# Performance work log

Measured on AMD Instinct MI355X. Metric: run time of the kernel, lower is better.

Reference implementation:

```python
import jax, jax.numpy as jnp
import numpy as np

B, S, D, H = 2, 2048, 1024, 16
DK = D // H  # 64


def setup_inputs() -> dict:
    key = jax.random.key(0)
    k0, k1, k2, k3, k4, k5, k6 = jax.random.split(key, 7)
    scale = 0.02
    return {
        "q": jax.random.normal(k0, (B, S, D), dtype=jnp.float32),
        "k": jax.random.normal(k1, (B, S, D), dtype=jnp.float32),
        "v": jax.random.normal(k2, (B, S, D), dtype=jnp.float32),
        # per-head Q/K projection weights (n_head separate Linear layers, bias=False)
        "Wq": jax.random.normal(k3, (H, D, DK), dtype=jnp.float32) * scale,
        "Wk": jax.random.normal(k4, (H, D, DK), dtype=jnp.float32) * scale,
        # shared V projection (the same v_layer object is reused for every head)
        "Wv": jax.random.normal(k5, (D, DK), dtype=jnp.float32) * scale,
        # output projection fc: d_v -> d_model, bias=False
        "Wo": jax.random.normal(k6, (DK, D), dtype=jnp.float32) * scale,
    }


def reference(q, k, v, Wq, Wk, Wv, Wo):
    d_k = Wq.shape[-1]
    # batched per-head projections (replaces the Python loop over heads)
    qs = jnp.einsum("bsd,hdk->bhsk", q, Wq)          # [B,H,S,DK]
    ks = jnp.einsum("bsd,hdk->bhsk", k, Wk)          # [B,H,S,DK]
    vs = jnp.einsum("bsd,dk->bsk", v, Wv)            # [B,S,DK] shared across heads
    scores = jnp.einsum("bhsk,bhtk->bhst", qs, ks) / jnp.sqrt(
        jnp.asarray(d_k, dtype=jnp.float32)
    )                                                 # [B,H,S,S]
    attn = jax.nn.softmax(scores, axis=-1)            # [B,H,S,S]; dropout = identity (eval)
    heads = jnp.einsum("bhst,btk->bhsk", attn, vs)    # [B,H,S,DK]
    head = heads.mean(axis=1)                         # mean over heads, not concat
    attn_mean = attn.mean(axis=1)                     # [B,S,S]
    out = jnp.einsum("bsk,kd->bsd", head, Wo)         # [B,S,D]; dropout = identity
    return (out, attn_mean)
```

## Files before the change

### kernel.cpp

```cpp
#include <hip/hip_runtime.h>

#define B_ 2
#define S_ 2048
#define D_ 1024
#define H_ 16
#define DK_ 64

typedef __bf16 bf8 __attribute__((ext_vector_type(8)));
typedef float f4 __attribute__((ext_vector_type(4)));
typedef unsigned short u16x8 __attribute__((ext_vector_type(8)));

__device__ __forceinline__ unsigned short f2bf_bits(float f) {
  unsigned int u = __float_as_uint(f);
  return (unsigned short)((u + 0x7fffu + ((u >> 16) & 1u)) >> 16);
}

__device__ __forceinline__ bf8 pack_bf8(f4 lo, f4 hi) {
  u16x8 u;
  u[0] = f2bf_bits(lo[0]); u[1] = f2bf_bits(lo[1]);
  u[2] = f2bf_bits(lo[2]); u[3] = f2bf_bits(lo[3]);
  u[4] = f2bf_bits(hi[0]); u[5] = f2bf_bits(hi[1]);
  u[6] = f2bf_bits(hi[2]); u[7] = f2bf_bits(hi[3]);
  union { u16x8 u; bf8 b; } x; x.u = u; return x.b;
}

__device__ __forceinline__ bf8 ldb(const unsigned short* p) {
  return *reinterpret_cast<const bf8*>(p);
}

__device__ __forceinline__ void stage16(const void* g, void* l) {
  __builtin_amdgcn_global_load_lds(
      (const __attribute__((address_space(1))) void*)g,
      (__attribute__((address_space(3))) void*)l, 16, 0, 0);
}

#define MFMA(a, b, c) __builtin_amdgcn_mfma_f32_16x16x32_bf16((a), (b), (c), 0, 0, 0)

__global__ void k_prep(const float* __restrict__ q, const float* __restrict__ k,
                       const float* __restrict__ wq, const float* __restrict__ wk,
                       const float* __restrict__ wv, const float* __restrict__ wo,
                       unsigned short* __restrict__ qb, unsigned short* __restrict__ kb,
                       unsigned short* __restrict__ wqt, unsigned short* __restrict__ wkt,
                       unsigned short* __restrict__ wvt, unsigned short* __restrict__ wot) {
  __shared__ float tl[64 * 65];
  int bid = blockIdx.x, tid = threadIdx.x;
  const int rr = tid >> 6, cc = tid & 63;
  if (bid < 4096) {
    int which = bid >> 11;
    long i = ((long)(bid & 2047) * 256 + tid) * 8;
    const float* src = which ? k : q;
    unsigned short* dst = which ? kb : qb;
    f4 lo = *reinterpret_cast<const f4*>(src + i);
    f4 hi = *reinterpret_cast<const f4*>(src + i + 4);
    *reinterpret_cast<bf8*>(dst + i) = pack_bf8(lo, hi);
  } else if (bid < 4352) {
    int blk = bid - 4096;
    int h = blk >> 4, d0 = (blk & 15) * 64;
    for (int m = 0; m < 2; ++m) {
      const float* src = m ? wk : wq;
      unsigned short* dst = m ? wkt : wqt;
      if (m) __syncthreads();
#pragma unroll
      for (int it = 0; it < 16; ++it) {
        int d = it * 4 + rr;
        tl[cc * 65 + d] = src[(long)h * 65536 + (d0 + d) * 64 + cc];
      }
      __syncthreads();
#pragma unroll
      for (int it = 0; it < 16; ++it) {
        int n = it * 4 + rr;
        dst[(long)h * 65536 + n * 1024 + d0 + cc] = f2bf_bits(tl[n * 65 + cc]);
      }
    }
  } else if (bid < 4368) {
    int d0 = (bid - 4352) * 64;
#pragma unroll
    for (int it = 0; it < 16; ++it) {
      int d = it * 4 + rr;
      tl[cc * 65 + d] = wv[(long)(d0 + d) * 64 + cc];
    }
    __syncthreads();
#pragma unroll
    for (int it = 0; it < 16; ++it) {
      int n = it * 4 + rr;
      wvt[(long)n * 1024 + d0 + cc] = f2bf_bits(tl[n * 65 + cc]);
    }
  } else {
    int d0 = (bid - 4368) * 64;
#pragma unroll
    for (int it = 0; it < 16; ++it) {
      int kk = it * 4 + rr;
      tl[cc * 65 + kk] = wo[(long)kk * 1024 + d0 + cc];
    }
    __syncthreads();
#pragma unroll
    for (int it = 0; it < 16; ++it) {
      int ddl = it * 4 + rr;
      wot[(long)(d0 + ddl) * 64 + cc] = f2bf_bits(tl[ddl * 65 + cc]);
    }
  }
}

__global__ __launch_bounds__(256) void k_gemm_qk(
    const unsigned short* __restrict__ qb, const unsigned short* __restrict__ kb,
    const unsigned short* __restrict__ wqt, const unsigned short* __restrict__ wkt,
    unsigned short* __restrict__ qsb, unsigned short* __restrict__ ksb) {
  __shared__ unsigned short lds[8192];
  const int tid = threadIdx.x, wave = tid >> 6, lane = tid & 63;
  const int l15 = lane & 15, quad = lane >> 4;
  const int m0 = blockIdx.x * 128, n0 = blockIdx.y * 128;
  const int which = blockIdx.z;
  const unsigned short* A = which ? kb : qb;
  const unsigned short* W = which ? wkt : wqt;
  unsigned short* C = which ? ksb : qsb;
  const float scale = which ? 1.0f : 0.18033688011112042f;
  const int wr = wave >> 1, wc = wave & 1;

  f4 acc[4][4];
#pragma unroll
  for (int i = 0; i < 4; ++i)
#pragma unroll
    for (int j = 0; j < 4; ++j) acc[i][j] = f4{0.f, 0.f, 0.f, 0.f};

  const int sl15 = tid & 15, squad = (tid >> 4) & 3, st = tid >> 6;
  const unsigned short* gA = A + (long)(m0 + st * 16 + sl15) * D_ + squad * 8;
  const unsigned short* gB = W + (long)(n0 + st * 16 + sl15) * D_ + squad * 8;

  for (int k0 = 0; k0 < D_; k0 += 32) {
    stage16(gA + k0, lds + tid * 8);
    stage16(gA + 64 * D_ + k0, lds + 2048 + tid * 8);
    stage16(gB + k0, lds + 4096 + tid * 8);
    stage16(gB + 64 * D_ + k0, lds + 6144 + tid * 8);
    __syncthreads();
    bf8 aF[4], bF[4];
#pragma unroll
    for (int mi = 0; mi < 4; ++mi)
      aF[mi] = ldb(lds + (wr * 4 + mi) * 512 + lane * 8);
#pragma unroll
    for (int ni = 0; ni < 4; ++ni)
      bF[ni] = ldb(lds + 4096 + (wc * 4 + ni) * 512 + lane * 8);
#pragma unroll
    for (int mi = 0; mi < 4; ++mi)
#pragma unroll
      for (int ni = 0; ni < 4; ++ni)
        acc[mi][ni] = MFMA(aF[mi], bF[ni], acc[mi][ni]);
    __syncthreads();
  }
#pragma unroll
  for (int mi = 0; mi < 4; ++mi)
#pragma unroll
    for (int r = 0; r < 4; ++r) {
      long row = m0 + wr * 64 + mi * 16 + quad * 4 + r;
#pragma unroll
      for (int ni = 0; ni < 4; ++ni)
        C[row * D_ + n0 + wc * 64 + ni * 16 + l15] = f2bf_bits(acc[mi][ni][r] * scale);
    }
}

__global__ __launch_bounds__(256) void k_pv(
    const float* __restrict__ v, const unsigned short* __restrict__ wvt,
    float* __restrict__ pv) {
  const int tid = threadIdx.x, wave = tid >> 6, lane = tid & 63;
  const int l15 = lane & 15, quad = lane >> 4;
  const int rg = blockIdx.x, kc = blockIdx.y;
  const int row0 = rg * 64 + wave * 16;
  const float* arow = v + (long)(row0 + l15) * D_ + kc * 256 + quad * 8;
  const unsigned short* wbase = wvt + kc * 256 + quad * 8;
  f4 acc[4];
  for (int i = 0; i < 4; ++i) acc[i] = f4{0.f, 0.f, 0.f, 0.f};
  for (int k0 = 0; k0 < 256; k0 += 32) {
    f4 alo = *reinterpret_cast<const f4*>(arow + k0);
    f4 ahi = *reinterpret_cast<const f4*>(arow + k0 + 4);
    bf8 a = pack_bf8(alo, ahi);
#pragma unroll
    for (int i = 0; i < 4; ++i) {
      bf8 bf = ldb(wbase + (long)(i * 16 + l15) * D_ + k0);
      acc[i] = MFMA(a, bf, acc[i]);
    }
  }
#pragma unroll
  for (int i = 0; i < 4; ++i)
#pragma unroll
    for (int r = 0; r < 4; ++r)
      pv[((long)kc * 4096 + row0 + quad * 4 + r) * 64 + i * 16 + l15] = acc[i][r];
}

__global__ void k_vred(const float* __restrict__ pv, unsigned short* __restrict__ vst) {
  int e = blockIdx.x * 256 + threadIdx.x;
  int t = e & 2047, dk = (e >> 11) & 63, b = e >> 17;
  long row = (long)b * S_ + t;
  float s = pv[row * 64 + dk] + pv[(4096 + row) * 64 + dk] +
            pv[(8192 + row) * 64 + dk] + pv[(12288 + row) * 64 + dk];
  vst[e] = f2bf_bits(s);
}

__global__ __launch_bounds__(512) void k_denom(
    const unsigned short* __restrict__ qsb, const unsigned short* __restrict__ ksb,
    float* __restrict__ recip) {
  __shared__ unsigned short lds[8192];
  const int tid = threadIdx.x, wave = tid >> 6, lane = tid & 63;
  const int l15 = lane & 15, quad = lane >> 4;
  const int stile = blockIdx.x, h = blockIdx.y, b = blockIdx.z;
  const int s0 = stile * 128 + wave * 16;

  const unsigned short* qrow = qsb + ((long)(b * S_) + s0 + l15) * D_ + h * 64 + quad * 8;
  bf8 a0 = ldb(qrow);
  bf8 a1 = ldb(qrow + 32);

  f4 sum = f4{0.f, 0.f, 0.f, 0.f};
  for (int t0 = 0; t0 < S_; t0 += 128) {
#pragma unroll
    for (int i = 0; i < 2; ++i) {
      int u = i * 512 + tid;
      int sl15 = u & 15, squad = (u >> 4) & 3, stt = (u >> 6) & 7, sh2 = u >> 9;
      stage16(ksb + ((long)(b * S_) + t0 + stt * 16 + sl15) * D_ + h * 64 + sh2 * 32 + squad * 8,
              lds + u * 8);
    }
    __syncthreads();
#pragma unroll
    for (int tt = 0; tt < 8; ++tt) {
      bf8 b0 = ldb(lds + tt * 512 + lane * 8);
      bf8 b1 = ldb(lds + 4096 + tt * 512 + lane * 8);
      f4 d = f4{0.f, 0.f, 0.f, 0.f};
      d = MFMA(a0, b0, d);
      d = MFMA(a1, b1, d);
#pragma unroll
      for (int r = 0; r < 4; ++r) sum[r] += __builtin_amdgcn_exp2f(d[r]);
    }
    __syncthreads();
  }
#pragma unroll
  for (int m = 1; m < 16; m <<= 1) {
#pragma unroll
    for (int r = 0; r < 4; ++r) sum[r] += __shfl_xor(sum[r], m, 64);
  }
  if (l15 == 0) {
    float* rp = recip + (long)(b * H_ + h) * S_ + s0 + quad * 4;
#pragma unroll
    for (int r = 0; r < 4; ++r) rp[r] = 1.0f / (16.0f * sum[r]);
  }
}

__global__ __launch_bounds__(512) void k_attn(
    const unsigned short* __restrict__ qsb, const unsigned short* __restrict__ ksb,
    const float* __restrict__ recip, float* __restrict__ am) {
  __shared__ unsigned short lds[8192];
  const int tid = threadIdx.x, wave = tid >> 6, lane = tid & 63;
  const int l15 = lane & 15, quad = lane >> 4;
  const int tchunk = blockIdx.x, stile = blockIdx.y, b = blockIdx.z;
  const int s0 = stile * 128 + wave * 16;
  const int t0c = tchunk * 128;

  f4 acc[8];
#pragma unroll
  for (int tt = 0; tt < 8; ++tt) acc[tt] = f4{0.f, 0.f, 0.f, 0.f};

  const unsigned short* qbase = qsb + ((long)(b * S_) + s0 + l15) * D_ + quad * 8;

  for (int h = 0; h < H_; ++h) {
#pragma unroll
    for (int i = 0; i < 2; ++i) {
      int u = i * 512 + tid;
      int sl15 = u & 15, squad = (u >> 4) & 3, stt = (u >> 6) & 7, sh2 = u >> 9;
      stage16(ksb + ((long)(b * S_) + t0c + stt * 16 + sl15) * D_ + h * 64 + sh2 * 32 + squad * 8,
              lds + u * 8);
    }
    bf8 a0 = ldb(qbase + h * 64);
    bf8 a1 = ldb(qbase + h * 64 + 32);
    f4 rp = *reinterpret_cast<const f4*>(recip + (long)(b * H_ + h) * S_ + s0 + quad * 4);
    __syncthreads();
#pragma unroll
    for (int tt = 0; tt < 8; ++tt) {
      bf8 b0 = ldb(lds + tt * 512 + lane * 8);
      bf8 b1 = ldb(lds + 4096 + tt * 512 + lane * 8);
      f4 d = f4{0.f, 0.f, 0.f, 0.f};
      d = MFMA(a0, b0, d);
      d = MFMA(a1, b1, d);
#pragma unroll
      for (int r = 0; r < 4; ++r) acc[tt][r] += rp[r] * __builtin_amdgcn_exp2f(d[r]);
    }
    __syncthreads();
  }
  float* obase = am + ((long)b * S_ + s0 + quad * 4) * S_ + t0c + l15;
#pragma unroll
  for (int tt = 0; tt < 8; ++tt)
#pragma unroll
    for (int r = 0; r < 4; ++r) obase[(long)r * S_ + tt * 16] = acc[tt][r];
}

__global__ __launch_bounds__(256) void k_hpart(
    const float* __restrict__ am, const unsigned short* __restrict__ vst,
    float* __restrict__ ph) {
  const int tid = threadIdx.x, wave = tid >> 6, lane = tid & 63;
  const int l15 = lane & 15, quad = lane >> 4;
  const int rg = blockIdx.x, kc = blockIdx.y;
  const int row0 = rg * 64 + wave * 16;
  const int b = row0 >> 11;
  const float* arow = am + (long)(row0 + l15) * S_ + kc * 512 + quad * 8;
  const unsigned short* vb = vst + (long)b * DK_ * S_ + kc * 512 + quad * 8;
  f4 acc[4];
  for (int i = 0; i < 4; ++i) acc[i] = f4{0.f, 0.f, 0.f, 0.f};
  for (int t0 = 0; t0 < 512; t0 += 32) {
    f4 alo = *reinterpret_cast<const f4*>(arow + t0);
    f4 ahi = *reinterpret_cast<const f4*>(arow + t0 + 4);
    bf8 a = pack_bf8(alo, ahi);
#pragma unroll
    for (int i = 0; i < 4; ++i) {
      bf8 bf = ldb(vb + (long)(i * 16 + l15) * S_ + t0);
      acc[i] = MFMA(a, bf, acc[i]);
    }
  }
#pragma unroll
  for (int i = 0; i < 4; ++i)
#pragma unroll
    for (int r = 0; r < 4; ++r)
      ph[((long)kc * 4096 + row0 + quad * 4 + r) * 64 + i * 16 + l15] = acc[i][r];
}

__global__ void k_hred(const float* __restrict__ ph, unsigned short* __restrict__ headb) {
  int e = blockIdx.x * 256 + threadIdx.x;
  float s = ph[e] + ph[e + 4096 * 64] + ph[e + 2 * 4096 * 64] + ph[e + 3 * 4096 * 64];
  headb[e] = f2bf_bits(s);
}

__global__ __launch_bounds__(256) void k_out(
    const unsigned short* __restrict__ head, const unsigned short* __restrict__ wot,
    float* __restrict__ out) {
  const int tid = threadIdx.x, wave = tid >> 6, lane = tid & 63;
  const int l15 = lane & 15, quad = lane >> 4;
  const int dchunk = blockIdx.x, stile = blockIdx.y, b = blockIdx.z;
  const int s0 = stile * 64 + wave * 16;
  const int n0 = dchunk * 128;
  const unsigned short* hrow = head + ((long)b * S_ + s0 + l15) * DK_ + quad * 8;
  bf8 a0 = ldb(hrow);
  bf8 a1 = ldb(hrow + 32);
  const unsigned short* wb = wot + quad * 8;
  float* obase = out + ((long)b * S_ + s0 + quad * 4) * D_ + n0 + l15;
#pragma unroll
  for (int i = 0; i < 8; ++i) {
    const unsigned short* wp = wb + (long)(n0 + i * 16 + l15) * DK_;
    bf8 b0 = ldb(wp);
    bf8 b1 = ldb(wp + 32);
    f4 d = f4{0.f, 0.f, 0.f, 0.f};
    d = MFMA(a0, b0, d);
    d = MFMA(a1, b1, d);
#pragma unroll
    for (int r = 0; r < 4; ++r) obase[(long)r * D_ + i * 16] = d[r];
  }
}

extern "C" void kernel_launch(void* const* d_in, const int* in_sizes, int n_in,
                              void* d_out, int out_size, void* d_ws, size_t ws_size,
                              hipStream_t stream) {
  const float* q  = (const float*)d_in[0];
  const float* k  = (const float*)d_in[1];
  const float* v  = (const float*)d_in[2];
  const float* Wq = (const float*)d_in[3];
  const float* Wk = (const float*)d_in[4];
  const float* Wv = (const float*)d_in[5];
  const float* Wo = (const float*)d_in[6];

  float* out = (float*)d_out;
  float* am  = out + (long)B_ * S_ * D_;

  unsigned short* qsb  = (unsigned short*)d_ws;
  unsigned short* ksb  = qsb + 4194304;
  unsigned short* wqt  = ksb + 4194304;
  unsigned short* wkt  = wqt + 1048576;
  unsigned short* wvt  = wkt + 1048576;
  unsigned short* wot  = wvt + 65536;
  unsigned short* vst  = wot + 65536;
  unsigned short* headb= vst + 262144;
  float* recip = (float*)(headb + 262144);

  unsigned short* qb = (unsigned short*)am;
  unsigned short* kb = qb + 4194304;
  float* part = out;

  k_prep<<<4384, 256, 0, stream>>>(q, k, Wq, Wk, Wv, Wo, qb, kb, wqt, wkt, wvt, wot);
  k_gemm_qk<<<dim3(32, 8, 2), 256, 0, stream>>>(qb, kb, wqt, wkt, qsb, ksb);
  k_pv<<<dim3(64, 4), 256, 0, stream>>>(v, wvt, part);
  k_vred<<<1024, 256, 0, stream>>>(part, vst);
  k_denom<<<dim3(16, 16, 2), 512, 0, stream>>>(qsb, ksb, recip);
  k_attn<<<dim3(16, 16, 2), 512, 0, stream>>>(qsb, ksb, recip, am);
  k_hpart<<<dim3(64, 4), 256, 0, stream>>>(am, vst, part);
  k_hred<<<1024, 256, 0, stream>>>(part, headb);
  k_out<<<dim3(8, 32, 2), 256, 0, stream>>>(headb, wot, out);
}
```

Measured before the change: 246.9 us.

## Double-buffer K tiles in attention kernels, widen GEMM K-step, split reductions finer

The denominator and attention kernels now use 256 threads with each wave covering 32 query rows, so each staged K fragment feeds two MFMA chains. They also double-buffer K tiles in LDS, prefetching the next head or t-chunk while computing the current one. The QK projection GEMM stages 64-wide K slices per barrier instead of 32, halving the number of syncs. The V-projection and head-partial kernels split the reduction into 8 chunks instead of 4 for more blocks, and the reducers sum 8 partials. The cost is higher register and LDS use per block and more partial-sum traffic.

```diff
diff --git a/kernel.cpp b/kernel.cpp
--- a/kernel.cpp
+++ b/kernel.cpp
@@ -105,7 +105,7 @@
     const unsigned short* __restrict__ qb, const unsigned short* __restrict__ kb,
     const unsigned short* __restrict__ wqt, const unsigned short* __restrict__ wkt,
     unsigned short* __restrict__ qsb, unsigned short* __restrict__ ksb) {
-  __shared__ unsigned short lds[8192];
+  __shared__ unsigned short lds[16384];
   const int tid = threadIdx.x, wave = tid >> 6, lane = tid & 63;
   const int l15 = lane & 15, quad = lane >> 4;
   const int m0 = blockIdx.x * 128, n0 = blockIdx.y * 128;
@@ -122,28 +122,31 @@
 #pragma unroll
     for (int j = 0; j < 4; ++j) acc[i][j] = f4{0.f, 0.f, 0.f, 0.f};
 
-  const int sl15 = tid & 15, squad = (tid >> 4) & 3, st = tid >> 6;
-  const unsigned short* gA = A + (long)(m0 + st * 16 + sl15) * D_ + squad * 8;
-  const unsigned short* gB = W + (long)(n0 + st * 16 + sl15) * D_ + squad * 8;
-
-  for (int k0 = 0; k0 < D_; k0 += 32) {
-    stage16(gA + k0, lds + tid * 8);
-    stage16(gA + 64 * D_ + k0, lds + 2048 + tid * 8);
-    stage16(gB + k0, lds + 4096 + tid * 8);
-    stage16(gB + 64 * D_ + k0, lds + 6144 + tid * 8);
-    __syncthreads();
-    bf8 aF[4], bF[4];
-#pragma unroll
-    for (int mi = 0; mi < 4; ++mi)
-      aF[mi] = ldb(lds + (wr * 4 + mi) * 512 + lane * 8);
-#pragma unroll
-    for (int ni = 0; ni < 4; ++ni)
-      bF[ni] = ldb(lds + 4096 + (wc * 4 + ni) * 512 + lane * 8);
-#pragma unroll
-    for (int mi = 0; mi < 4; ++mi)
+  for (int k0 = 0; k0 < D_; k0 += 64) {
+#pragma unroll
+    for (int i = 0; i < 4; ++i) {
+      int u = i * 256 + tid;
+      int T = u >> 6, rg = T & 7, kh = T >> 3, sl15 = u & 15, squad = (u >> 4) & 3;
+      stage16(A + (long)(m0 + rg * 16 + sl15) * D_ + k0 + kh * 32 + squad * 8, lds + u * 8);
+      stage16(W + (long)(n0 + rg * 16 + sl15) * D_ + k0 + kh * 32 + squad * 8,
+              lds + 8192 + u * 8);
+    }
+    __syncthreads();
+#pragma unroll
+    for (int kh = 0; kh < 2; ++kh) {
+      bf8 aF[4], bF[4];
+#pragma unroll
+      for (int mi = 0; mi < 4; ++mi)
+        aF[mi] = ldb(lds + (wr * 4 + mi + 8 * kh) * 512 + lane * 8);
 #pragma unroll
       for (int ni = 0; ni < 4; ++ni)
-        acc[mi][ni] = MFMA(aF[mi], bF[ni], acc[mi][ni]);
+        bF[ni] = ldb(lds + 8192 + (wc * 4 + ni + 8 * kh) * 512 + lane * 8);
+#pragma unroll
+      for (int mi = 0; mi < 4; ++mi)
+#pragma unroll
+        for (int ni = 0; ni < 4; ++ni)
+          acc[mi][ni] = MFMA(aF[mi], bF[ni], acc[mi][ni]);
+    }
     __syncthreads();
   }
 #pragma unroll
@@ -164,11 +167,12 @@
   const int l15 = lane & 15, quad = lane >> 4;
   const int rg = blockIdx.x, kc = blockIdx.y;
   const int row0 = rg * 64 + wave * 16;
-  const float* arow = v + (long)(row0 + l15) * D_ + kc * 256 + quad * 8;
-  const unsigned short* wbase = wvt + kc * 256 + quad * 8;
+  const float* arow = v + (long)(row0 + l15) * D_ + kc * 128 + quad * 8;
+  const unsigned short* wbase = wvt + kc * 128 + quad * 8;
   f4 acc[4];
   for (int i = 0; i < 4; ++i) acc[i] = f4{0.f, 0.f, 0.f, 0.f};
-  for (int k0 = 0; k0 < 256; k0 += 32) {
+#pragma unroll
+  for (int k0 = 0; k0 < 128; k0 += 32) {
     f4 alo = *reinterpret_cast<const f4*>(arow + k0);
     f4 ahi = *reinterpret_cast<const f4*>(arow + k0 + 4);
     bf8 a = pack_bf8(alo, ahi);
@@ -189,103 +193,157 @@
   int e = blockIdx.x * 256 + threadIdx.x;
   int t = e & 2047, dk = (e >> 11) & 63, b = e >> 17;
   long row = (long)b * S_ + t;
-  float s = pv[row * 64 + dk] + pv[(4096 + row) * 64 + dk] +
-            pv[(8192 + row) * 64 + dk] + pv[(12288 + row) * 64 + dk];
+  float s = 0.f;
+#pragma unroll
+  for (int c = 0; c < 8; ++c) s += pv[((long)c * 4096 + row) * 64 + dk];
   vst[e] = f2bf_bits(s);
 }
 
-__global__ __launch_bounds__(512) void k_denom(
+__global__ __launch_bounds__(256) void k_denom(
     const unsigned short* __restrict__ qsb, const unsigned short* __restrict__ ksb,
     float* __restrict__ recip) {
-  __shared__ unsigned short lds[8192];
+  __shared__ unsigned short lds[16384];
   const int tid = threadIdx.x, wave = tid >> 6, lane = tid & 63;
   const int l15 = lane & 15, quad = lane >> 4;
   const int stile = blockIdx.x, h = blockIdx.y, b = blockIdx.z;
-  const int s0 = stile * 128 + wave * 16;
-
-  const unsigned short* qrow = qsb + ((long)(b * S_) + s0 + l15) * D_ + h * 64 + quad * 8;
-  bf8 a0 = ldb(qrow);
-  bf8 a1 = ldb(qrow + 32);
-
-  f4 sum = f4{0.f, 0.f, 0.f, 0.f};
-  for (int t0 = 0; t0 < S_; t0 += 128) {
-#pragma unroll
-    for (int i = 0; i < 2; ++i) {
-      int u = i * 512 + tid;
-      int sl15 = u & 15, squad = (u >> 4) & 3, stt = (u >> 6) & 7, sh2 = u >> 9;
-      stage16(ksb + ((long)(b * S_) + t0 + stt * 16 + sl15) * D_ + h * 64 + sh2 * 32 + squad * 8,
-              lds + u * 8);
-    }
-    __syncthreads();
+  const int sw = stile * 128 + wave * 32;
+
+  const unsigned short* qrow0 = qsb + ((long)(b * S_) + sw + l15) * D_ + h * 64 + quad * 8;
+  bf8 a0 = ldb(qrow0);
+  bf8 a1 = ldb(qrow0 + 32);
+  bf8 a2 = ldb(qrow0 + 16 * D_);
+  bf8 a3 = ldb(qrow0 + 16 * D_ + 32);
+
+  f4 sum0 = f4{0.f, 0.f, 0.f, 0.f}, sum1 = f4{0.f, 0.f, 0.f, 0.f};
+
+  const long kbase = (long)(b * S_);
+#pragma unroll
+  for (int i = 0; i < 4; ++i) {
+    int u = i * 256 + tid;
+    int T = u >> 6, sl15 = u & 15, squad = (u >> 4) & 3;
+    stage16(ksb + (kbase + (T & 7) * 16 + sl15) * D_ + h * 64 + (T >> 3) * 32 + squad * 8,
+            lds + u * 8);
+  }
+  for (int it = 0; it < 16; ++it) {
+    __syncthreads();
+    if (it < 15) {
+      int t0n = (it + 1) * 128, bufn = (it + 1) & 1;
+#pragma unroll
+      for (int i = 0; i < 4; ++i) {
+        int u = i * 256 + tid;
+        int T = u >> 6, sl15 = u & 15, squad = (u >> 4) & 3;
+        stage16(ksb + (kbase + t0n + (T & 7) * 16 + sl15) * D_ + h * 64 + (T >> 3) * 32 + squad * 8,
+                lds + bufn * 8192 + u * 8);
+      }
+    }
+    const unsigned short* L = lds + (it & 1) * 8192;
 #pragma unroll
     for (int tt = 0; tt < 8; ++tt) {
-      bf8 b0 = ldb(lds + tt * 512 + lane * 8);
-      bf8 b1 = ldb(lds + 4096 + tt * 512 + lane * 8);
-      f4 d = f4{0.f, 0.f, 0.f, 0.f};
-      d = MFMA(a0, b0, d);
-      d = MFMA(a1, b1, d);
-#pragma unroll
-      for (int r = 0; r < 4; ++r) sum[r] += __builtin_amdgcn_exp2f(d[r]);
-    }
-    __syncthreads();
+      bf8 b0 = ldb(L + tt * 512 + lane * 8);
+      bf8 b1 = ldb(L + 4096 + tt * 512 + lane * 8);
+      f4 d0 = f4{0.f, 0.f, 0.f, 0.f};
+      d0 = MFMA(a0, b0, d0);
+      d0 = MFMA(a1, b1, d0);
+      f4 d1 = f4{0.f, 0.f, 0.f, 0.f};
+      d1 = MFMA(a2, b0, d1);
+      d1 = MFMA(a3, b1, d1);
+#pragma unroll
+      for (int r = 0; r < 4; ++r) {
+        sum0[r] += __builtin_amdgcn_exp2f(d0[r]);
+        sum1[r] += __builtin_amdgcn_exp2f(d1[r]);
+      }
+    }
   }
 #pragma unroll
   for (int m = 1; m < 16; m <<= 1) {
 #pragma unroll
-    for (int r = 0; r < 4; ++r) sum[r] += __shfl_xor(sum[r], m, 64);
+    for (int r = 0; r < 4; ++r) {
+      sum0[r] += __shfl_xor(sum0[r], m, 64);
+      sum1[r] += __shfl_xor(sum1[r], m, 64);
+    }
   }
   if (l15 == 0) {
-    float* rp = recip + (long)(b * H_ + h) * S_ + s0 + quad * 4;
-#pragma unroll
-    for (int r = 0; r < 4; ++r) rp[r] = 1.0f / (16.0f * sum[r]);
-  }
-}
-
-__global__ __launch_bounds__(512) void k_attn(
+    float* rp0 = recip + (long)(b * H_ + h) * S_ + sw + quad * 4;
+#pragma unroll
+    for (int r = 0; r < 4; ++r) {
+      rp0[r] = 1.0f / (16.0f * sum0[r]);
+      rp0[16 + r] = 1.0f / (16.0f * sum1[r]);
+    }
+  }
+}
+
+__global__ __launch_bounds__(256) void k_attn(
     const unsigned short* __restrict__ qsb, const unsigned short* __restrict__ ksb,
     const float* __restrict__ recip, float* __restrict__ am) {
-  __shared__ unsigned short lds[8192];
+  __shared__ unsigned short lds[16384];
   const int tid = threadIdx.x, wave = tid >> 6, lane = tid & 63;
   const int l15 = lane & 15, quad = lane >> 4;
   const int tchunk = blockIdx.x, stile = blockIdx.y, b = blockIdx.z;
-  const int s0 = stile * 128 + wave * 16;
+  const int sw = stile * 128 + wave * 32;
   const int t0c = tchunk * 128;
 
-  f4 acc[8];
-#pragma unroll
-  for (int tt = 0; tt < 8; ++tt) acc[tt] = f4{0.f, 0.f, 0.f, 0.f};
-
-  const unsigned short* qbase = qsb + ((long)(b * S_) + s0 + l15) * D_ + quad * 8;
-
+  f4 acc0[8], acc1[8];
+#pragma unroll
+  for (int tt = 0; tt < 8; ++tt) {
+    acc0[tt] = f4{0.f, 0.f, 0.f, 0.f};
+    acc1[tt] = f4{0.f, 0.f, 0.f, 0.f};
+  }
+
+  const unsigned short* qrow0 = qsb + ((long)(b * S_) + sw + l15) * D_ + quad * 8;
+  const long kbase = (long)(b * S_) + t0c;
+
+#pragma unroll
+  for (int i = 0; i < 4; ++i) {
+    int u = i * 256 + tid;
+    int T = u >> 6, sl15 = u & 15, squad = (u >> 4) & 3;
+    stage16(ksb + (kbase + (T & 7) * 16 + sl15) * D_ + (T >> 3) * 32 + squad * 8, lds + u * 8);
+  }
   for (int h = 0; h < H_; ++h) {
-#pragma unroll
-    for (int i = 0; i < 2; ++i) {
-      int u = i * 512 + tid;
-      int sl15 = u & 15, squad = (u >> 4) & 3, stt = (u >> 6) & 7, sh2 = u >> 9;
-      stage16(ksb + ((long)(b * S_) + t0c + stt * 16 + sl15) * D_ + h * 64 + sh2 * 32 + squad * 8,
-              lds + u * 8);
-    }
-    bf8 a0 = ldb(qbase + h * 64);
-    bf8 a1 = ldb(qbase + h * 64 + 32);
-    f4 rp = *reinterpret_cast<const f4*>(recip + (long)(b * H_ + h) * S_ + s0 + quad * 4);
-    __syncthreads();
+    __syncthreads();
+    if (h < 15) {
+      int bufn = (h + 1) & 1;
+#pragma unroll
+      for (int i = 0; i < 4; ++i) {
+        int u = i * 256 + tid;
+        int T = u >> 6, sl15 = u & 15, squad = (u >> 4) & 3;
+        stage16(ksb + (kbase + (T & 7) * 16 + sl15) * D_ + (h + 1) * 64 + (T >> 3) * 32 + squad * 8,
+                lds + bufn * 8192 + u * 8);
+      }
+    }
+    const unsigned short* L = lds + (h & 1) * 8192;
+    bf8 a0 = ldb(qrow0 + h * 64);
+    bf8 a1 = ldb(qrow0 + h * 64 + 32);
+    bf8 a2 = ldb(qrow0 + 16 * D_ + h * 64);
+    bf8 a3 = ldb(qrow0 + 16 * D_ + h * 64 + 32);
+    const float* rpp = recip + (long)(b * H_ + h) * S_ + sw + quad * 4;
+    f4 rp0 = *reinterpret_cast<const f4*>(rpp);
+    f4 rp1 = *reinterpret_cast<const f4*>(rpp + 16);
 #pragma unroll
     for (int tt = 0; tt < 8; ++tt) {
-      bf8 b0 = ldb(lds + tt * 512 + lane * 8);
-      bf8 b1 = ldb(lds + 4096 + tt * 512 + lane * 8);
-      f4 d = f4{0.f, 0.f, 0.f, 0.f};
-      d = MFMA(a0, b0, d);
-      d = MFMA(a1, b1, d);
-#pragma unroll
-      for (int r = 0; r < 4; ++r) acc[tt][r] += rp[r] * __builtin_amdgcn_exp2f(d[r]);
-    }
-    __syncthreads();
-  }
-  float* obase = am + ((long)b * S_ + s0 + quad * 4) * S_ + t0c + l15;
+      bf8 b0 = ldb(L + tt * 512 + lane * 8);
+      bf8 b1 = ldb(L + 4096 + tt * 512 + lane * 8);
+      f4 d0 = f4{0.f, 0.f, 0.f, 0.f};
+      d0 = MFMA(a0, b0, d0);
+      d0 = MFMA(a1, b1, d0);
+      f4 d1 = f4{0.f, 0.f, 0.f, 0.f};
+      d1 = MFMA(a2, b0, d1);
+      d1 = MFMA(a3, b1, d1);
+#pragma unroll
+      for (int r = 0; r < 4; ++r) {
+        acc0[tt][r] += rp0[r] * __builtin_amdgcn_exp2f(d0[r]);
+        acc1[tt][r] += rp1[r] * __builtin_amdgcn_exp2f(d1[r]);
+      }
+    }
+  }
+  float* ob0 = am + ((long)b * S_ + sw + quad * 4) * S_ + t0c + l15;
+  float* ob1 = ob0 + 16 * S_;
 #pragma unroll
   for (int tt = 0; tt < 8; ++tt)
 #pragma unroll
-    for (int r = 0; r < 4; ++r) obase[(long)r * S_ + tt * 16] = acc[tt][r];
+    for (int r = 0; r < 4; ++r) {
+      ob0[(long)r * S_ + tt * 16] = acc0[tt][r];
+      ob1[(long)r * S_ + tt * 16] = acc1[tt][r];
+    }
 }
 
 __global__ __launch_bounds__(256) void k_hpart(
@@ -296,11 +354,12 @@
   const int rg = blockIdx.x, kc = blockIdx.y;
   const int row0 = rg * 64 + wave * 16;
   const int b = row0 >> 11;
-  const float* arow = am + (long)(row0 + l15) * S_ + kc * 512 + quad * 8;
-  const unsigned short* vb = vst + (long)b * DK_ * S_ + kc * 512 + quad * 8;
+  const float* arow = am + (long)(row0 + l15) * S_ + kc * 256 + quad * 8;
+  const unsigned short* vb = vst + (long)b * DK_ * S_ + kc * 256 + quad * 8;
   f4 acc[4];
   for (int i = 0; i < 4; ++i) acc[i] = f4{0.f, 0.f, 0.f, 0.f};
-  for (int t0 = 0; t0 < 512; t0 += 32) {
+#pragma unroll
+  for (int t0 = 0; t0 < 256; t0 += 32) {
     f4 alo = *reinterpret_cast<const f4*>(arow + t0);
     f4 ahi = *reinterpret_cast<const f4*>(arow + t0 + 4);
     bf8 a = pack_bf8(alo, ahi);
@@ -319,7 +378,9 @@
 
 __global__ void k_hred(const float* __restrict__ ph, unsigned short* __restrict__ headb) {
   int e = blockIdx.x * 256 + threadIdx.x;
-  float s = ph[e] + ph[e + 4096 * 64] + ph[e + 2 * 4096 * 64] + ph[e + 3 * 4096 * 64];
+  float s = 0.f;
+#pragma unroll
+  for (int c = 0; c < 8; ++c) s += ph[(long)c * 262144 + e];
   headb[e] = f2bf_bits(s);
 }
 
@@ -379,11 +440,11 @@
 
   k_prep<<<4384, 256, 0, stream>>>(q, k, Wq, Wk, Wv, Wo, qb, kb, wqt, wkt, wvt, wot);
   k_gemm_qk<<<dim3(32, 8, 2), 256, 0, stream>>>(qb, kb, wqt, wkt, qsb, ksb);
-  k_pv<<<dim3(64, 4), 256, 0, stream>>>(v, wvt, part);
+  k_pv<<<dim3(64, 8), 256, 0, stream>>>(v, wvt, part);
   k_vred<<<1024, 256, 0, stream>>>(part, vst);
-  k_denom<<<dim3(16, 16, 2), 512, 0, stream>>>(qsb, ksb, recip);
-  k_attn<<<dim3(16, 16, 2), 512, 0, stream>>>(qsb, ksb, recip, am);
-  k_hpart<<<dim3(64, 4), 256, 0, stream>>>(am, vst, part);
+  k_denom<<<dim3(16, 16, 2), 256, 0, stream>>>(qsb, ksb, recip);
+  k_attn<<<dim3(16, 16, 2), 256, 0, stream>>>(qsb, ksb, recip, am);
+  k_hpart<<<dim3(64, 8), 256, 0, stream>>>(am, vst, part);
   k_hred<<<1024, 256, 0, stream>>>(part, headb);
   k_out<<<dim3(8, 32, 2), 256, 0, stream>>>(headb, wot, out);
 }
```

Result: slower. 258.9 us (+4.9%).

## Double-buffer K tiles in attention kernels, deepen GEMM k-step, split reductions finer

Applied to the files above, without the earlier changes.

The denominator and attention kernels now double-buffer the K tiles in LDS, prefetching the next tile (and, in attention, the next head's Q fragments and reciprocals) while computing the current one, with one barrier per iteration instead of two. The QK projection GEMM stages a 64-wide k slice per barrier, which halves the number of syncs. The V-projection and head partial-sum kernels split the reduction dimension into 8 chunks instead of 4 to launch more blocks, and the reduction kernels sum 8 partials. These changes target barrier stalls, memory latency and low occupancy, at the cost of more LDS per block and more partial-sum traffic.

```diff
diff --git a/kernel.cpp b/kernel.cpp
--- a/kernel.cpp
+++ b/kernel.cpp
@@ -105,7 +105,7 @@
     const unsigned short* __restrict__ qb, const unsigned short* __restrict__ kb,
     const unsigned short* __restrict__ wqt, const unsigned short* __restrict__ wkt,
     unsigned short* __restrict__ qsb, unsigned short* __restrict__ ksb) {
-  __shared__ unsigned short lds[8192];
+  __shared__ unsigned short lds[16384];
   const int tid = threadIdx.x, wave = tid >> 6, lane = tid & 63;
   const int l15 = lane & 15, quad = lane >> 4;
   const int m0 = blockIdx.x * 128, n0 = blockIdx.y * 128;
@@ -122,28 +122,31 @@
 #pragma unroll
     for (int j = 0; j < 4; ++j) acc[i][j] = f4{0.f, 0.f, 0.f, 0.f};
 
-  const int sl15 = tid & 15, squad = (tid >> 4) & 3, st = tid >> 6;
-  const unsigned short* gA = A + (long)(m0 + st * 16 + sl15) * D_ + squad * 8;
-  const unsigned short* gB = W + (long)(n0 + st * 16 + sl15) * D_ + squad * 8;
-
-  for (int k0 = 0; k0 < D_; k0 += 32) {
-    stage16(gA + k0, lds + tid * 8);
-    stage16(gA + 64 * D_ + k0, lds + 2048 + tid * 8);
-    stage16(gB + k0, lds + 4096 + tid * 8);
-    stage16(gB + 64 * D_ + k0, lds + 6144 + tid * 8);
-    __syncthreads();
-    bf8 aF[4], bF[4];
-#pragma unroll
-    for (int mi = 0; mi < 4; ++mi)
-      aF[mi] = ldb(lds + (wr * 4 + mi) * 512 + lane * 8);
-#pragma unroll
-    for (int ni = 0; ni < 4; ++ni)
-      bF[ni] = ldb(lds + 4096 + (wc * 4 + ni) * 512 + lane * 8);
-#pragma unroll
-    for (int mi = 0; mi < 4; ++mi)
+  for (int k0 = 0; k0 < D_; k0 += 64) {
+#pragma unroll
+    for (int i = 0; i < 4; ++i) {
+      int u = i * 256 + tid;
+      int T = u >> 6, rg = T & 7, kh = T >> 3, sl15 = u & 15, squad = (u >> 4) & 3;
+      stage16(A + (long)(m0 + rg * 16 + sl15) * D_ + k0 + kh * 32 + squad * 8, lds + u * 8);
+      stage16(W + (long)(n0 + rg * 16 + sl15) * D_ + k0 + kh * 32 + squad * 8,
+              lds + 8192 + u * 8);
+    }
+    __syncthreads();
+#pragma unroll
+    for (int kh = 0; kh < 2; ++kh) {
+      bf8 aF[4], bF[4];
+#pragma unroll
+      for (int mi = 0; mi < 4; ++mi)
+        aF[mi] = ldb(lds + (wr * 4 + mi + 8 * kh) * 512 + lane * 8);
 #pragma unroll
       for (int ni = 0; ni < 4; ++ni)
-        acc[mi][ni] = MFMA(aF[mi], bF[ni], acc[mi][ni]);
+        bF[ni] = ldb(lds + 8192 + (wc * 4 + ni + 8 * kh) * 512 + lane * 8);
+#pragma unroll
+      for (int mi = 0; mi < 4; ++mi)
+#pragma unroll
+        for (int ni = 0; ni < 4; ++ni)
+          acc[mi][ni] = MFMA(aF[mi], bF[ni], acc[mi][ni]);
+    }
     __syncthreads();
   }
 #pragma unroll
@@ -164,11 +167,12 @@
   const int l15 = lane & 15, quad = lane >> 4;
   const int rg = blockIdx.x, kc = blockIdx.y;
   const int row0 = rg * 64 + wave * 16;
-  const float* arow = v + (long)(row0 + l15) * D_ + kc * 256 + quad * 8;
-  const unsigned short* wbase = wvt + kc * 256 + quad * 8;
+  const float* arow = v + (long)(row0 + l15) * D_ + kc * 128 + quad * 8;
+  const unsigned short* wbase = wvt + kc * 128 + quad * 8;
   f4 acc[4];
   for (int i = 0; i < 4; ++i) acc[i] = f4{0.f, 0.f, 0.f, 0.f};
-  for (int k0 = 0; k0 < 256; k0 += 32) {
+#pragma unroll
+  for (int k0 = 0; k0 < 128; k0 += 32) {
     f4 alo = *reinterpret_cast<const f4*>(arow + k0);
     f4 ahi = *reinterpret_cast<const f4*>(arow + k0 + 4);
     bf8 a = pack_bf8(alo, ahi);
@@ -189,15 +193,16 @@
   int e = blockIdx.x * 256 + threadIdx.x;
   int t = e & 2047, dk = (e >> 11) & 63, b = e >> 17;
   long row = (long)b * S_ + t;
-  float s = pv[row * 64 + dk] + pv[(4096 + row) * 64 + dk] +
-            pv[(8192 + row) * 64 + dk] + pv[(12288 + row) * 64 + dk];
+  float s = 0.f;
+#pragma unroll
+  for (int c = 0; c < 8; ++c) s += pv[((long)c * 4096 + row) * 64 + dk];
   vst[e] = f2bf_bits(s);
 }
 
 __global__ __launch_bounds__(512) void k_denom(
     const unsigned short* __restrict__ qsb, const unsigned short* __restrict__ ksb,
     float* __restrict__ recip) {
-  __shared__ unsigned short lds[8192];
+  __shared__ unsigned short lds[16384];
   const int tid = threadIdx.x, wave = tid >> 6, lane = tid & 63;
   const int l15 = lane & 15, quad = lane >> 4;
   const int stile = blockIdx.x, h = blockIdx.y, b = blockIdx.z;
@@ -207,27 +212,37 @@
   bf8 a0 = ldb(qrow);
   bf8 a1 = ldb(qrow + 32);
 
+  const int sl15 = tid & 15, squad = (tid >> 4) & 3;
+  const unsigned short* gk[2];
+#pragma unroll
+  for (int i = 0; i < 2; ++i) {
+    int u = i * 512 + tid;
+    int rg = (u >> 6) & 7, kh = u >> 9;
+    gk[i] = ksb + ((long)(b * S_) + rg * 16 + sl15) * D_ + h * 64 + kh * 32 + squad * 8;
+  }
+#pragma unroll
+  for (int i = 0; i < 2; ++i) stage16(gk[i], lds + (i * 512 + tid) * 8);
+
   f4 sum = f4{0.f, 0.f, 0.f, 0.f};
-  for (int t0 = 0; t0 < S_; t0 += 128) {
-#pragma unroll
-    for (int i = 0; i < 2; ++i) {
-      int u = i * 512 + tid;
-      int sl15 = u & 15, squad = (u >> 4) & 3, stt = (u >> 6) & 7, sh2 = u >> 9;
-      stage16(ksb + ((long)(b * S_) + t0 + stt * 16 + sl15) * D_ + h * 64 + sh2 * 32 + squad * 8,
-              lds + u * 8);
-    }
-    __syncthreads();
+  for (int it = 0; it < 16; ++it) {
+    __syncthreads();
+    if (it < 15) {
+      int bufn = (it + 1) & 1;
+#pragma unroll
+      for (int i = 0; i < 2; ++i)
+        stage16(gk[i] + (long)(it + 1) * 128 * D_, lds + bufn * 8192 + (i * 512 + tid) * 8);
+    }
+    const unsigned short* L = lds + (it & 1) * 8192;
 #pragma unroll
     for (int tt = 0; tt < 8; ++tt) {
-      bf8 b0 = ldb(lds + tt * 512 + lane * 8);
-      bf8 b1 = ldb(lds + 4096 + tt * 512 + lane * 8);
+      bf8 b0 = ldb(L + tt * 512 + lane * 8);
+      bf8 b1 = ldb(L + 4096 + tt * 512 + lane * 8);
       f4 d = f4{0.f, 0.f, 0.f, 0.f};
       d = MFMA(a0, b0, d);
       d = MFMA(a1, b1, d);
 #pragma unroll
       for (int r = 0; r < 4; ++r) sum[r] += __builtin_amdgcn_exp2f(d[r]);
     }
-    __syncthreads();
   }
 #pragma unroll
   for (int m = 1; m < 16; m <<= 1) {
@@ -244,7 +259,7 @@
 __global__ __launch_bounds__(512) void k_attn(
     const unsigned short* __restrict__ qsb, const unsigned short* __restrict__ ksb,
     const float* __restrict__ recip, float* __restrict__ am) {
-  __shared__ unsigned short lds[8192];
+  __shared__ unsigned short lds[16384];
   const int tid = threadIdx.x, wave = tid >> 6, lane = tid & 63;
   const int l15 = lane & 15, quad = lane >> 4;
   const int tchunk = blockIdx.x, stile = blockIdx.y, b = blockIdx.z;
@@ -255,31 +270,50 @@
 #pragma unroll
   for (int tt = 0; tt < 8; ++tt) acc[tt] = f4{0.f, 0.f, 0.f, 0.f};
 
-  const unsigned short* qbase = qsb + ((long)(b * S_) + s0 + l15) * D_ + quad * 8;
+  const unsigned short* qrow = qsb + ((long)(b * S_) + s0 + l15) * D_ + quad * 8;
+  const float* rbase = recip + (long)b * H_ * S_ + s0 + quad * 4;
+
+  const int sl15 = tid & 15, squad = (tid >> 4) & 3;
+  const unsigned short* gk[2];
+#pragma unroll
+  for (int i = 0; i < 2; ++i) {
+    int u = i * 512 + tid;
+    int rg = (u >> 6) & 7, kh = u >> 9;
+    gk[i] = ksb + ((long)(b * S_) + t0c + rg * 16 + sl15) * D_ + kh * 32 + squad * 8;
+  }
+#pragma unroll
+  for (int i = 0; i < 2; ++i) stage16(gk[i], lds + (i * 512 + tid) * 8);
+
+  bf8 a0 = ldb(qrow);
+  bf8 a1 = ldb(qrow + 32);
+  f4 rp = *reinterpret_cast<const f4*>(rbase);
 
   for (int h = 0; h < H_; ++h) {
-#pragma unroll
-    for (int i = 0; i < 2; ++i) {
-      int u = i * 512 + tid;
-      int sl15 = u & 15, squad = (u >> 4) & 3, stt = (u >> 6) & 7, sh2 = u >> 9;
-      stage16(ksb + ((long)(b * S_) + t0c + stt * 16 + sl15) * D_ + h * 64 + sh2 * 32 + squad * 8,
-              lds + u * 8);
-    }
-    bf8 a0 = ldb(qbase + h * 64);
-    bf8 a1 = ldb(qbase + h * 64 + 32);
-    f4 rp = *reinterpret_cast<const f4*>(recip + (long)(b * H_ + h) * S_ + s0 + quad * 4);
-    __syncthreads();
+    __syncthreads();
+    if (h < 15) {
+      int bufn = (h + 1) & 1;
+#pragma unroll
+      for (int i = 0; i < 2; ++i)
+        stage16(gk[i] + (h + 1) * 64, lds + bufn * 8192 + (i * 512 + tid) * 8);
+    }
+    bf8 a0c = a0, a1c = a1;
+    f4 rpc = rp;
+    if (h < 15) {
+      a0 = ldb(qrow + (h + 1) * 64);
+      a1 = ldb(qrow + (h + 1) * 64 + 32);
+      rp = *reinterpret_cast<const f4*>(rbase + (long)(h + 1) * S_);
+    }
+    const unsigned short* L = lds + (h & 1) * 8192;
 #pragma unroll
     for (int tt = 0; tt < 8; ++tt) {
-      bf8 b0 = ldb(lds + tt * 512 + lane * 8);
-      bf8 b1 = ldb(lds + 4096 + tt * 512 + lane * 8);
+      bf8 b0 = ldb(L + tt * 512 + lane * 8);
+      bf8 b1 = ldb(L + 4096 + tt * 512 + lane * 8);
       f4 d = f4{0.f, 0.f, 0.f, 0.f};
-      d = MFMA(a0, b0, d);
-      d = MFMA(a1, b1, d);
-#pragma unroll
-      for (int r = 0; r < 4; ++r) acc[tt][r] += rp[r] * __builtin_amdgcn_exp2f(d[r]);
-    }
-    __syncthreads();
+      d = MFMA(a0c, b0, d);
+      d = MFMA(a1c, b1, d);
+#pragma unroll
+      for (int r = 0; r < 4; ++r) acc[tt][r] += rpc[r] * __builtin_amdgcn_exp2f(d[r]);
+    }
   }
   float* obase = am + ((long)b * S_ + s0 + quad * 4) * S_ + t0c + l15;
 #pragma unroll
@@ -296,11 +330,12 @@
   const int rg = blockIdx.x, kc = blockIdx.y;
   const int row0 = rg * 64 + wave * 16;
   const int b = row0 >> 11;
-  const float* arow = am + (long)(row0 + l15) * S_ + kc * 512 + quad * 8;
-  const unsigned short* vb = vst + (long)b * DK_ * S_ + kc * 512 + quad * 8;
+  const float* arow = am + (long)(row0 + l15) * S_ + kc * 256 + quad * 8;
+  const unsigned short* vb = vst + (long)b * DK_ * S_ + kc * 256 + quad * 8;
   f4 acc[4];
   for (int i = 0; i < 4; ++i) acc[i] = f4{0.f, 0.f, 0.f, 0.f};
-  for (int t0 = 0; t0 < 512; t0 += 32) {
+#pragma unroll
+  for (int t0 = 0; t0 < 256; t0 += 32) {
     f4 alo = *reinterpret_cast<const f4*>(arow + t0);
     f4 ahi = *reinterpret_cast<const f4*>(arow + t0 + 4);
     bf8 a = pack_bf8(alo, ahi);
@@ -319,7 +354,9 @@
 
 __global__ void k_hred(const float* __restrict__ ph, unsigned short* __restrict__ headb) {
   int e = blockIdx.x * 256 + threadIdx.x;
-  float s = ph[e] + ph[e + 4096 * 64] + ph[e + 2 * 4096 * 64] + ph[e + 3 * 4096 * 64];
+  float s = 0.f;
+#pragma unroll
+  for (int c = 0; c < 8; ++c) s += ph[(long)c * 262144 + e];
   headb[e] = f2bf_bits(s);
 }
 
@@ -379,11 +416,11 @@
 
   k_prep<<<4384, 256, 0, stream>>>(q, k, Wq, Wk, Wv, Wo, qb, kb, wqt, wkt, wvt, wot);
   k_gemm_qk<<<dim3(32, 8, 2), 256, 0, stream>>>(qb, kb, wqt, wkt, qsb, ksb);
-  k_pv<<<dim3(64, 4), 256, 0, stream>>>(v, wvt, part);
+  k_pv<<<dim3(64, 8), 256, 0, stream>>>(v, wvt, part);
   k_vred<<<1024, 256, 0, stream>>>(part, vst);
   k_denom<<<dim3(16, 16, 2), 512, 0, stream>>>(qsb, ksb, recip);
   k_attn<<<dim3(16, 16, 2), 512, 0, stream>>>(qsb, ksb, recip, am);
-  k_hpart<<<dim3(64, 4), 256, 0, stream>>>(am, vst, part);
+  k_hpart<<<dim3(64, 8), 256, 0, stream>>>(am, vst, part);
   k_hred<<<1024, 256, 0, stream>>>(part, headb);
   k_out<<<dim3(8, 32, 2), 256, 0, stream>>>(headb, wot, out);
 }
```

After: 248.6 us. No clear change (+0.7%).
